# Kernel tuning notes

Hardware: AMD Instinct MI355X
Metric: run time of the kernel (lower is better)

## Reference

```python
import jax, jax.numpy as jnp
import numpy as np

# --- dims (match init_kwargs) ---
B, IN_DIM, OUT_DIM, CAUSES_DIM = 4096, 512, 4096, 256
POOL = 2
N_STEPS = 10
GAMMA = 0.1
LR = 0.001  # fixed lr inside _IstaStep
S = int(np.sqrt(OUT_DIM))   # 64: side of the square code map
SP = S // POOL              # 32: pooled side
POOLED_DIM = SP * SP        # 1024: second dim of V (pool path)


def setup_inputs() -> dict:
    key = jax.random.key(0)
    k1, k2, k3 = jax.random.split(key, 3)
    inputs = jax.random.normal(k1, (B, IN_DIM), jnp.float32)
    limit = float(np.sqrt(6.0 / (OUT_DIM + IN_DIM)))  # glorot_uniform for W
    W = jax.random.uniform(k2, (OUT_DIM, IN_DIM), jnp.float32, -limit, limit)
    # pool_flag=True -> V ~ U(0, 1) with shape (causes_dim, pooled_dim)
    V = jax.random.uniform(k3, (CAUSES_DIM, POOLED_DIM), jnp.float32, 0.0, 1.0)
    return {"inputs": inputs, "W": W, "V": V}


def _soft_threshold(x, t):
    # _proxOp: max(x - t, 0) + min(x + t, 0)
    return jnp.maximum(x - t, 0.0) + jnp.minimum(x + t, 0.0)


def reference(inputs, W, V):
    Bn = inputs.shape[0]
    x0 = jnp.zeros((Bn, OUT_DIM), inputs.dtype)
    u0 = jnp.full((Bn, CAUSES_DIM), 0.1, inputs.dtype)   # zeros + 0.1
    rec0 = jnp.zeros((Bn, IN_DIM), inputs.dtype)

    def step(carry, _):
        x, u, _rec = carry
        outputs = x @ W                                   # [B, IN_DIM], linear activation
        # NOTE: original uses (1 + exp(-z)) * 0.5 (not a true sigmoid) — keep faithful
        causes = (1.0 + jnp.exp(-(u @ V))) * 0.5          # [B, POOLED_DIM]
        # nearest-neighbor upsample of the pooled cause map back to the code map
        causes_up = jnp.repeat(
            jnp.repeat(causes.reshape(Bn, SP, SP), POOL, axis=1), POOL, axis=2
        ).reshape(Bn, OUT_DIM)                            # [B, OUT_DIM]
        # T.grad(sum((inputs - x@W)^2), x) = 2 * (x@W - inputs) @ W.T
        grad_x = 2.0 * (outputs - inputs) @ W.T           # [B, OUT_DIM]
        # prior=0 in _get_output, so the _proxInnov branch is dead code
        x_new = jax.lax.stop_gradient(                    # disconnected_grad
            _soft_threshold(x - LR * grad_x, LR * GAMMA * causes_up))
        # 2x2 max pool over the square code map
        x_pool = x_new.reshape(Bn, SP, POOL, SP, POOL).max(axis=(2, 4)).reshape(Bn, POOLED_DIM)
        # T.grad(sum(causes(u) * x_pool * gamma), u): d causes/dz = -0.5*exp(-z)
        dcauses = -0.5 * jnp.exp(-(u @ V))                # [B, POOLED_DIM]
        grad_u = (dcauses * x_pool * GAMMA) @ V.T         # [B, CAUSES_DIM]
        u_new = jax.lax.stop_gradient(
            _soft_threshold(u - LR * grad_u, LR * GAMMA / 10.0))
        return (x_new, u_new, outputs), None

    (x, u, rec), _ = jax.lax.scan(step, (x0, u0, rec0), None, length=N_STEPS)
    # return_mode='rec': reconstruction computed in the last step (from x_{T-1})
    return rec
```

## Files before the change

kernel.cpp:

```cpp
#include <hip/hip_runtime.h>
#include <math.h>


#define NB 4096
#define IN_DIM 512
#define OUT_DIM 4096
#define CAUSES_DIM 256
#define POOLED_DIM 1024

typedef __attribute__((ext_vector_type(8))) short short8;
typedef __attribute__((ext_vector_type(4))) float f32x4;

static constexpr float LR = 0.001f;
static constexpr float GAMMA = 0.1f;

enum { EP_R = 0, EP_OUT, EP_UUP };

__device__ __forceinline__ float softthr(float v, float t) {
    return fmaxf(v - t, 0.0f) + fminf(v + t, 0.0f);
}
__device__ __forceinline__ unsigned short f2bf(float f) {
    unsigned int u = __builtin_bit_cast(unsigned int, f);
    u = (u + 0x7fffu + ((u >> 16) & 1u)) >> 16;
    return (unsigned short)u;
}
__device__ __forceinline__ float bf2f(unsigned short h) {
    return __builtin_bit_cast(float, (unsigned int)h << 16);
}
__device__ __forceinline__ void gload_lds16(const unsigned short* g, unsigned short* l) {
    __builtin_amdgcn_global_load_lds(
        (const __attribute__((address_space(1))) void*)g,
        (__attribute__((address_space(3))) void*)l, 16, 0, 0);
}

template<int ROWS, int K>
__device__ __forceinline__ void stage_tile(const unsigned short* __restrict__ g,
                                           unsigned short* l, int row0, int k0, int t)
{
#pragma unroll
    for (int j = 0; j < ROWS / 32; j++) {
        const int idx = j * 256 + t;
        const int row = idx >> 3;
        const int sl  = (idx & 7) ^ (row & 7);
        gload_lds16(g + (size_t)(row0 + row) * K + k0 + sl * 8,
                    l + (size_t)(idx & ~63) * 8);
    }
}

template<int BM, int BN, int K>
__device__ __forceinline__ void kloop(unsigned short* lds,
    const unsigned short* __restrict__ A, const unsigned short* __restrict__ B,
    int m0, int n0, f32x4 (&acc)[BM / 32][BN / 32])
{
    constexpr int FM = BM / 32, FN = BN / 32;
    constexpr int NK = K / 64, ST = (BM + BN) * 64, L = (BM + BN) / 32;
    static_assert(NK >= 3, "pipeline needs >=3 K-tiles");
    const int t = threadIdx.x;
    const int lane = t & 63, wid = t >> 6;
    const int l15 = lane & 15, l7 = lane & 7, g = lane >> 4;
    const int wm0 = (wid >> 1) * (BM / 2), wn0 = (wid & 1) * (BN / 2);

    auto stage = [&](int s, int b) {
        stage_tile<BM, K>(A, lds + b * ST, m0, s * 64, t);
        stage_tile<BN, K>(B, lds + b * ST + BM * 64, n0, s * 64, t);
    };
    auto comp = [&](int b) {
        const unsigned short* As = lds + b * ST;
        const unsigned short* Bs = lds + b * ST + BM * 64;
#pragma unroll
        for (int ks = 0; ks < 2; ks++) {
            const int so = (((ks * 4) + g) ^ l7) * 8;
            short8 af[FM], bfv[FN];
#pragma unroll
            for (int fi = 0; fi < FM; fi++)
                af[fi] = *(const short8*)&As[(wm0 + fi * 16 + l15) * 64 + so];
#pragma unroll
            for (int fj = 0; fj < FN; fj++)
                bfv[fj] = *(const short8*)&Bs[(wn0 + fj * 16 + l15) * 64 + so];
#pragma unroll
            for (int fi = 0; fi < FM; fi++)
#pragma unroll
                for (int fj = 0; fj < FN; fj++)
                    acc[fi][fj] = __builtin_amdgcn_mfma_f32_16x16x32_bf16(
                        af[fi], bfv[fj], acc[fi][fj], 0, 0, 0);
        }
    };

    stage(0, 0); stage(1, 1); stage(2, 2);
    int b = 0;
#pragma unroll 1
    for (int i = 0; i < NK - 2; ++i) {
        asm volatile("s_waitcnt vmcnt(%0)" :: "n"(2 * L) : "memory");
        __builtin_amdgcn_s_barrier();
        comp(b);
        __builtin_amdgcn_s_barrier();
        if (i + 3 < NK) stage(i + 3, b);
        b = (b == 2) ? 0 : b + 1;
    }
    asm volatile("s_waitcnt vmcnt(%0)" :: "n"(L) : "memory");
    __builtin_amdgcn_s_barrier();
    comp(b);
    b = (b == 2) ? 0 : b + 1;
    asm volatile("s_waitcnt vmcnt(0)" ::: "memory");
    __builtin_amdgcn_s_barrier();
    comp(b);
}

template<int BM, int BN, int N, int K, int EP>
__device__ void gemm_core(unsigned short* lds, int bid,
                          const unsigned short* __restrict__ A,
                          const unsigned short* __restrict__ B,
                          const float* __restrict__ auxf,
                          void* __restrict__ out0, void* __restrict__ out1)
{
    constexpr int FM = BM / 32, FN = BN / 32;
    constexpr int NX = N / BN, NWG = (NB / BM) * NX;
    const int t = threadIdx.x, lane = t & 63, wid = t >> 6;
    const int l15 = lane & 15, g = lane >> 4;
    const int work = ((bid & 7) * (NWG / 8)) + (bid >> 3);
    const int bn = work % NX, bm = work / NX;
    const int m0 = bm * BM, n0 = bn * BN;
    const int wm0 = (wid >> 1) * (BM / 2), wn0 = (wid & 1) * (BN / 2);

    f32x4 acc[FM][FN];
#pragma unroll
    for (int fi = 0; fi < FM; fi++)
#pragma unroll
        for (int fj = 0; fj < FN; fj++) acc[fi][fj] = (f32x4){0.f, 0.f, 0.f, 0.f};

    kloop<BM, BN, K>(lds, A, B, m0, n0, acc);

#pragma unroll
    for (int fi = 0; fi < FM; fi++) {
#pragma unroll
        for (int fj = 0; fj < FN; fj++) {
#pragma unroll
            for (int r = 0; r < 4; r++) {
                const int row = m0 + wm0 + fi * 16 + g * 4 + r;
                const int col = n0 + wn0 + fj * 16 + l15;
                const float v = acc[fi][fj][r];
                if (EP == EP_R) {
                    ((unsigned short*)out0)[(size_t)row * N + col] =
                        f2bf(v - auxf[(size_t)row * N + col]);
                } else if (EP == EP_OUT) {
                    ((float*)out0)[(size_t)row * N + col] = v;
                } else {
                    float* up = (float*)out0;
                    const size_t idx = (size_t)row * CAUSES_DIM + col;
                    const float uv = softthr(up[idx] - LR * v, LR * GAMMA * 0.1f);
                    up[idx] = uv;
                    ((unsigned short*)out1)[idx] = f2bf(uv);
                }
            }
        }
    }
}

template<bool FIRST, bool POOLF>
__global__ __launch_bounds__(256)
void xupc_kernel(const unsigned short* __restrict__ Rbf,
                 const unsigned short* __restrict__ Wbf,
                 const unsigned short* __restrict__ ubf,
                 const unsigned short* __restrict__ VTbf,
                 unsigned short* __restrict__ xbf,
                 unsigned short* __restrict__ gbf)
{
    constexpr int BM = 64, BN = 128;
    constexpr int NX = OUT_DIM / BN;
    constexpr int NWG = (NB / BM) * NX;
    __shared__ unsigned short lds[3 * (BM + BN) * 64 + 4096];
    unsigned* czdc = (unsigned*)(lds + 3 * (BM + BN) * 64);
    unsigned short* xs = lds;

    const int t = threadIdx.x, lane = t & 63, wid = t >> 6;
    const int l15 = lane & 15, g = lane >> 4;
    const int work = ((blockIdx.x & 7) * (NWG / 8)) + (blockIdx.x >> 3);
    const int bn = work % NX, bm = work / NX;
    const int m0 = bm * BM, n0 = bn * BN;
    const int wm0 = (wid >> 1) * 32, wn0 = (wid & 1) * 64;

    f32x4 acc[2][4];
#pragma unroll
    for (int fi = 0; fi < 2; fi++)
#pragma unroll
        for (int fj = 0; fj < 4; fj++) acc[fi][fj] = (f32x4){0.f, 0.f, 0.f, 0.f};
    kloop<64, 128, IN_DIM>(lds, Rbf, Wbf, m0, n0, acc);
    __syncthreads();

    f32x4 zacc[2][1];
    zacc[0][0] = (f32x4){0.f, 0.f, 0.f, 0.f};
    zacc[1][0] = (f32x4){0.f, 0.f, 0.f, 0.f};
    kloop<64, 32, CAUSES_DIM>(lds, ubf, VTbf, m0, bn * 32, zacc);

    {
        const int zc = (wid & 1) * 16 + l15;
#pragma unroll
        for (int fi = 0; fi < 2; fi++) {
#pragma unroll
            for (int r = 0; r < 4; r++) {
                const int zr = (wid >> 1) * 32 + fi * 16 + g * 4 + r;
                const float e = expf(-zacc[fi][0][r]);
                czdc[zr * 32 + zc] =
                    (unsigned)f2bf(0.5f + 0.5f * e) | ((unsigned)f2bf(-0.5f * e) << 16);
            }
        }
    }
    __syncthreads();

#pragma unroll
    for (int fi = 0; fi < 2; fi++) {
#pragma unroll
        for (int fj = 0; fj < 4; fj++) {
#pragma unroll
            for (int r = 0; r < 4; r++) {
                const int rloc = wm0 + fi * 16 + g * 4 + r;
                const int cloc = wn0 + fj * 16 + l15;
                const int pl = (cloc & 63) >> 1;
                const float cz = bf2f((unsigned short)(czdc[rloc * 32 + pl] & 0xffffu));
                const size_t idx = (size_t)(m0 + rloc) * OUT_DIM + n0 + cloc;
                const float xold = FIRST ? 0.0f : bf2f(xbf[idx]);
                const float xv = softthr(xold - 2.0f * LR * acc[fi][fj][r],
                                         LR * GAMMA * cz);
                const unsigned short xq = f2bf(xv);
                xbf[idx] = xq;
                if (POOLF) xs[rloc * 130 + cloc] = xq;
            }
        }
    }

    if (POOLF) {
        __syncthreads();
        const int p = t & 31;
        const int rbase = (t >> 5) * 8;
#pragma unroll
        for (int i = 0; i < 8; i++) {
            const int prow = rbase + i;
            const unsigned short* xr = &xs[prow * 130 + 2 * p];
            const float mx = fmaxf(fmaxf(bf2f(xr[0]), bf2f(xr[1])),
                                   fmaxf(bf2f(xr[64]), bf2f(xr[65])));
            const float dcv = bf2f((unsigned short)(czdc[prow * 32 + p] >> 16));
            gbf[(size_t)(m0 + prow) * POOLED_DIM + bn * 32 + p] = f2bf(dcv * mx * GAMMA);
        }
    }
}

__global__ __launch_bounds__(256)
void h_uup_r_kernel(const unsigned short* __restrict__ gbf,
                    const unsigned short* __restrict__ Vbf,
                    float* __restrict__ u, unsigned short* __restrict__ ubf,
                    const unsigned short* __restrict__ xbf,
                    const unsigned short* __restrict__ WTbf,
                    const float* __restrict__ inputs,
                    unsigned short* __restrict__ Rbf)
{
    __shared__ unsigned short lds[3 * (128 + 64) * 64];
    if (blockIdx.x < 256) {
        gemm_core<128, 64, IN_DIM, OUT_DIM, EP_R>(
            lds, blockIdx.x, xbf, WTbf, inputs, Rbf, nullptr);
    } else {
        gemm_core<64, 64, CAUSES_DIM, POOLED_DIM, EP_UUP>(
            lds, blockIdx.x - 256, gbf, Vbf, nullptr, u, ubf);
    }
}

__global__ __launch_bounds__(256)
void out_kernel(const unsigned short* __restrict__ xbf,
                const unsigned short* __restrict__ WTbf,
                float* __restrict__ out)
{
    __shared__ unsigned short lds[3 * (128 + 64) * 64];
    gemm_core<128, 64, IN_DIM, OUT_DIM, EP_OUT>(
        lds, blockIdx.x, xbf, WTbf, nullptr, out, nullptr);
}

__global__ __launch_bounds__(256)
void prep_k(const float* __restrict__ in, unsigned short* __restrict__ direct,
            unsigned short* __restrict__ transp, int R, int C)
{
    __shared__ float tile[32][33];
    const int bx = blockIdx.x * 32, by = blockIdx.y * 32;
    const int tx = threadIdx.x % 32, ty = threadIdx.x / 32;
#pragma unroll
    for (int i = 0; i < 32; i += 8) {
        const float v = in[(size_t)(by + ty + i) * C + bx + tx];
        tile[ty + i][tx] = v;
        direct[(size_t)(by + ty + i) * C + bx + tx] = f2bf(v);
    }
    __syncthreads();
#pragma unroll
    for (int i = 0; i < 32; i += 8)
        transp[(size_t)(bx + ty + i) * R + by + tx] = f2bf(tile[tx][ty + i]);
}

__global__ void negcast_k(const float* __restrict__ in, unsigned short* __restrict__ out,
                          int n4)
{
    const int i = blockIdx.x * 256 + threadIdx.x;
    if (i >= n4) return;
    float4 v = ((const float4*)in)[i];
    union { unsigned short s[4]; unsigned long long u; } p;
    p.s[0] = f2bf(-v.x); p.s[1] = f2bf(-v.y); p.s[2] = f2bf(-v.z); p.s[3] = f2bf(-v.w);
    ((unsigned long long*)out)[i] = p.u;
}

__global__ void fill_u_k(float* __restrict__ u, unsigned short* __restrict__ ubf, int n) {
    const int i = blockIdx.x * 256 + threadIdx.x;
    if (i >= n) return;
    u[i] = 0.1f;
    ubf[i] = f2bf(0.1f);
}

extern "C" void kernel_launch(void* const* d_in, const int* in_sizes, int n_in,
                              void* d_out, int out_size, void* d_ws, size_t ws_size,
                              hipStream_t stream)
{
    const float* inputs = (const float*)d_in[0];
    const float* W      = (const float*)d_in[1];
    const float* V      = (const float*)d_in[2];
    float* out = (float*)d_out;

    char* w = (char*)d_ws;
    unsigned short* xbf  = (unsigned short*)w; w += (size_t)NB * OUT_DIM * 2;
    unsigned short* Rbf  = (unsigned short*)w; w += (size_t)NB * IN_DIM * 2;
    unsigned short* gbf  = (unsigned short*)w; w += (size_t)NB * POOLED_DIM * 2;
    float*          u    = (float*)w;          w += (size_t)NB * CAUSES_DIM * 4;
    unsigned short* ubf  = (unsigned short*)w; w += (size_t)NB * CAUSES_DIM * 2;
    unsigned short* Wbf  = (unsigned short*)w; w += (size_t)OUT_DIM * IN_DIM * 2;
    unsigned short* WTbf = (unsigned short*)w; w += (size_t)OUT_DIM * IN_DIM * 2;
    unsigned short* Vbf  = (unsigned short*)w; w += (size_t)CAUSES_DIM * POOLED_DIM * 2;
    unsigned short* VTbf = (unsigned short*)w;

    prep_k<<<dim3(IN_DIM / 32, OUT_DIM / 32), 256, 0, stream>>>(W, Wbf, WTbf, OUT_DIM, IN_DIM);
    prep_k<<<dim3(POOLED_DIM / 32, CAUSES_DIM / 32), 256, 0, stream>>>(V, Vbf, VTbf, CAUSES_DIM, POOLED_DIM);
    fill_u_k<<<NB * CAUSES_DIM / 256, 256, 0, stream>>>(u, ubf, NB * CAUSES_DIM);
    negcast_k<<<NB * IN_DIM / 4 / 256, 256, 0, stream>>>(inputs, Rbf, NB * IN_DIM / 4);

    xupc_kernel<true, true><<<2048, 256, 0, stream>>>(Rbf, Wbf, ubf, VTbf, xbf, gbf);
    h_uup_r_kernel<<<512, 256, 0, stream>>>(gbf, Vbf, u, ubf, xbf, WTbf, inputs, Rbf);
    for (int t = 1; t < 8; t++) {
        xupc_kernel<false, true><<<2048, 256, 0, stream>>>(Rbf, Wbf, ubf, VTbf, xbf, gbf);
        h_uup_r_kernel<<<512, 256, 0, stream>>>(gbf, Vbf, u, ubf, xbf, WTbf, inputs, Rbf);
    }
    xupc_kernel<false, false><<<2048, 256, 0, stream>>>(Rbf, Wbf, ubf, VTbf, xbf, gbf);
    out_kernel<<<256, 256, 0, stream>>>(xbf, WTbf, out);
}
```

Measured before the change: 849.0 us.

## Enlarge xupc tile to 128x128, use double-buffered K pipeline, remap block tiles

The fused x-update kernel now computes 128x128 output tiles instead of 64x128, halving the grid and doubling per-block reuse of the W tiles and the cause tiles. All GEMM K-loops switch from a three-stage to a two-stage LDS pipeline to cut shared memory use. Block-to-tile mapping is changed to an XCD-aware grouped layout for xupc and a plain row-major layout for the other GEMMs. The risks are less latency hiding from the shallower pipeline, higher register pressure from the larger accumulator, and fewer blocks to fill the GPU.

Result: faster. 819.6 us (-3.5%).

```diff
diff --git a/kernel.cpp b/kernel.cpp
--- a/kernel.cpp
+++ b/kernel.cpp
@@ -48,13 +48,13 @@
 }
 
 template<int BM, int BN, int K>
-__device__ __forceinline__ void kloop(unsigned short* lds,
+__device__ __forceinline__ void kloop2(unsigned short* lds,
     const unsigned short* __restrict__ A, const unsigned short* __restrict__ B,
     int m0, int n0, f32x4 (&acc)[BM / 32][BN / 32])
 {
     constexpr int FM = BM / 32, FN = BN / 32;
     constexpr int NK = K / 64, ST = (BM + BN) * 64, L = (BM + BN) / 32;
-    static_assert(NK >= 3, "pipeline needs >=3 K-tiles");
+    static_assert(NK >= 2, "pipeline needs >=2 K-tiles");
     const int t = threadIdx.x;
     const int lane = t & 63, wid = t >> 6;
     const int l15 = lane & 15, l7 = lane & 7, g = lane >> 4;
@@ -86,40 +86,32 @@
         }
     };
 
-    stage(0, 0); stage(1, 1); stage(2, 2);
+    stage(0, 0); stage(1, 1);
     int b = 0;
 #pragma unroll 1
-    for (int i = 0; i < NK - 2; ++i) {
-        asm volatile("s_waitcnt vmcnt(%0)" :: "n"(2 * L) : "memory");
+    for (int i = 0; i < NK - 1; ++i) {
+        asm volatile("s_waitcnt vmcnt(%0)" :: "n"(L) : "memory");
         __builtin_amdgcn_s_barrier();
         comp(b);
         __builtin_amdgcn_s_barrier();
-        if (i + 3 < NK) stage(i + 3, b);
-        b = (b == 2) ? 0 : b + 1;
-    }
-    asm volatile("s_waitcnt vmcnt(%0)" :: "n"(L) : "memory");
-    __builtin_amdgcn_s_barrier();
-    comp(b);
-    b = (b == 2) ? 0 : b + 1;
+        if (i + 2 < NK) stage(i + 2, b);
+        b ^= 1;
+    }
     asm volatile("s_waitcnt vmcnt(0)" ::: "memory");
     __builtin_amdgcn_s_barrier();
     comp(b);
 }
 
 template<int BM, int BN, int N, int K, int EP>
-__device__ void gemm_core(unsigned short* lds, int bid,
+__device__ void gemm_core(unsigned short* lds, int m0, int n0,
                           const unsigned short* __restrict__ A,
                           const unsigned short* __restrict__ B,
                           const float* __restrict__ auxf,
                           void* __restrict__ out0, void* __restrict__ out1)
 {
     constexpr int FM = BM / 32, FN = BN / 32;
-    constexpr int NX = N / BN, NWG = (NB / BM) * NX;
     const int t = threadIdx.x, lane = t & 63, wid = t >> 6;
     const int l15 = lane & 15, g = lane >> 4;
-    const int work = ((bid & 7) * (NWG / 8)) + (bid >> 3);
-    const int bn = work % NX, bm = work / NX;
-    const int m0 = bm * BM, n0 = bn * BN;
     const int wm0 = (wid >> 1) * (BM / 2), wn0 = (wid & 1) * (BN / 2);
 
     f32x4 acc[FM][FN];
@@ -128,7 +120,7 @@
 #pragma unroll
         for (int fj = 0; fj < FN; fj++) acc[fi][fj] = (f32x4){0.f, 0.f, 0.f, 0.f};
 
-    kloop<BM, BN, K>(lds, A, B, m0, n0, acc);
+    kloop2<BM, BN, K>(lds, A, B, m0, n0, acc);
 
 #pragma unroll
     for (int fi = 0; fi < FM; fi++) {
@@ -165,40 +157,39 @@
                  unsigned short* __restrict__ xbf,
                  unsigned short* __restrict__ gbf)
 {
-    constexpr int BM = 64, BN = 128;
-    constexpr int NX = OUT_DIM / BN;
-    constexpr int NWG = (NB / BM) * NX;
-    __shared__ unsigned short lds[3 * (BM + BN) * 64 + 4096];
-    unsigned* czdc = (unsigned*)(lds + 3 * (BM + BN) * 64);
+    constexpr int BM = 128, BN = 128;
+    __shared__ unsigned short lds[2 * (BM + BN) * 64 + 8192];
+    unsigned* czdc = (unsigned*)(lds + 2 * (BM + BN) * 64);
     unsigned short* xs = lds;
 
     const int t = threadIdx.x, lane = t & 63, wid = t >> 6;
     const int l15 = lane & 15, g = lane >> 4;
-    const int work = ((blockIdx.x & 7) * (NWG / 8)) + (blockIdx.x >> 3);
-    const int bn = work % NX, bm = work / NX;
+    const int xcd = blockIdx.x & 7, l = blockIdx.x >> 3;
+    const int g2 = l >> 5, r2 = l & 31;
+    const int bm = g2 * 8 + (r2 >> 2), bn = xcd * 4 + (r2 & 3);
     const int m0 = bm * BM, n0 = bn * BN;
-    const int wm0 = (wid >> 1) * 32, wn0 = (wid & 1) * 64;
-
-    f32x4 acc[2][4];
-#pragma unroll
-    for (int fi = 0; fi < 2; fi++)
+    const int wm0 = (wid >> 1) * 64, wn0 = (wid & 1) * 64;
+
+    f32x4 acc[4][4];
+#pragma unroll
+    for (int fi = 0; fi < 4; fi++)
 #pragma unroll
         for (int fj = 0; fj < 4; fj++) acc[fi][fj] = (f32x4){0.f, 0.f, 0.f, 0.f};
-    kloop<64, 128, IN_DIM>(lds, Rbf, Wbf, m0, n0, acc);
+    kloop2<128, 128, IN_DIM>(lds, Rbf, Wbf, m0, n0, acc);
     __syncthreads();
 
-    f32x4 zacc[2][1];
-    zacc[0][0] = (f32x4){0.f, 0.f, 0.f, 0.f};
-    zacc[1][0] = (f32x4){0.f, 0.f, 0.f, 0.f};
-    kloop<64, 32, CAUSES_DIM>(lds, ubf, VTbf, m0, bn * 32, zacc);
+    f32x4 zacc[4][1];
+#pragma unroll
+    for (int fi = 0; fi < 4; fi++) zacc[fi][0] = (f32x4){0.f, 0.f, 0.f, 0.f};
+    kloop2<128, 32, CAUSES_DIM>(lds, ubf, VTbf, m0, bn * 32, zacc);
 
     {
         const int zc = (wid & 1) * 16 + l15;
 #pragma unroll
-        for (int fi = 0; fi < 2; fi++) {
+        for (int fi = 0; fi < 4; fi++) {
 #pragma unroll
             for (int r = 0; r < 4; r++) {
-                const int zr = (wid >> 1) * 32 + fi * 16 + g * 4 + r;
+                const int zr = (wid >> 1) * 64 + fi * 16 + g * 4 + r;
                 const float e = expf(-zacc[fi][0][r]);
                 czdc[zr * 32 + zc] =
                     (unsigned)f2bf(0.5f + 0.5f * e) | ((unsigned)f2bf(-0.5f * e) << 16);
@@ -208,7 +199,7 @@
     __syncthreads();
 
 #pragma unroll
-    for (int fi = 0; fi < 2; fi++) {
+    for (int fi = 0; fi < 4; fi++) {
 #pragma unroll
         for (int fj = 0; fj < 4; fj++) {
 #pragma unroll
@@ -231,9 +222,9 @@
     if (POOLF) {
         __syncthreads();
         const int p = t & 31;
-        const int rbase = (t >> 5) * 8;
-#pragma unroll
-        for (int i = 0; i < 8; i++) {
+        const int rbase = (t >> 5) * 16;
+#pragma unroll
+        for (int i = 0; i < 16; i++) {
             const int prow = rbase + i;
             const unsigned short* xr = &xs[prow * 130 + 2 * p];
             const float mx = fmaxf(fmaxf(bf2f(xr[0]), bf2f(xr[1])),
@@ -253,13 +244,15 @@
                     const float* __restrict__ inputs,
                     unsigned short* __restrict__ Rbf)
 {
-    __shared__ unsigned short lds[3 * (128 + 64) * 64];
+    __shared__ unsigned short lds[2 * (128 + 64) * 64];
     if (blockIdx.x < 256) {
+        const int bid = blockIdx.x;
         gemm_core<128, 64, IN_DIM, OUT_DIM, EP_R>(
-            lds, blockIdx.x, xbf, WTbf, inputs, Rbf, nullptr);
+            lds, (bid >> 3) * 128, (bid & 7) * 64, xbf, WTbf, inputs, Rbf, nullptr);
     } else {
+        const int bid = blockIdx.x - 256;
         gemm_core<64, 64, CAUSES_DIM, POOLED_DIM, EP_UUP>(
-            lds, blockIdx.x - 256, gbf, Vbf, nullptr, u, ubf);
+            lds, (bid >> 2) * 64, (bid & 3) * 64, gbf, Vbf, nullptr, u, ubf);
     }
 }
 
@@ -268,9 +261,10 @@
                 const unsigned short* __restrict__ WTbf,
                 float* __restrict__ out)
 {
-    __shared__ unsigned short lds[3 * (128 + 64) * 64];
+    __shared__ unsigned short lds[2 * (128 + 64) * 64];
+    const int bid = blockIdx.x;
     gemm_core<128, 64, IN_DIM, OUT_DIM, EP_OUT>(
-        lds, blockIdx.x, xbf, WTbf, nullptr, out, nullptr);
+        lds, (bid >> 3) * 128, (bid & 7) * 64, xbf, WTbf, nullptr, out, nullptr);
 }
 
 __global__ __launch_bounds__(256)
@@ -335,12 +329,12 @@
     fill_u_k<<<NB * CAUSES_DIM / 256, 256, 0, stream>>>(u, ubf, NB * CAUSES_DIM);
     negcast_k<<<NB * IN_DIM / 4 / 256, 256, 0, stream>>>(inputs, Rbf, NB * IN_DIM / 4);
 
-    xupc_kernel<true, true><<<2048, 256, 0, stream>>>(Rbf, Wbf, ubf, VTbf, xbf, gbf);
+    xupc_kernel<true, true><<<1024, 256, 0, stream>>>(Rbf, Wbf, ubf, VTbf, xbf, gbf);
     h_uup_r_kernel<<<512, 256, 0, stream>>>(gbf, Vbf, u, ubf, xbf, WTbf, inputs, Rbf);
     for (int t = 1; t < 8; t++) {
-        xupc_kernel<false, true><<<2048, 256, 0, stream>>>(Rbf, Wbf, ubf, VTbf, xbf, gbf);
+        xupc_kernel<false, true><<<1024, 256, 0, stream>>>(Rbf, Wbf, ubf, VTbf, xbf, gbf);
         h_uup_r_kernel<<<512, 256, 0, stream>>>(gbf, Vbf, u, ubf, xbf, WTbf, inputs, Rbf);
     }
-    xupc_kernel<false, false><<<2048, 256, 0, stream>>>(Rbf, Wbf, ubf, VTbf, xbf, gbf);
+    xupc_kernel<false, false><<<1024, 256, 0, stream>>>(Rbf, Wbf, ubf, VTbf, xbf, gbf);
     out_kernel<<<256, 256, 0, stream>>>(xbf, WTbf, out);
 }
```
